# Performance work log

Hardware: AMD Instinct MI355X
Metric: run time of the kernel (lower is better)

The kernel has to match this reference:

```python
import jax, jax.numpy as jnp
import numpy as np

ITERS = 3  # iteration_num in the original module
B, L, H, N_LABELS = 16, 64, 512, 64


def setup_inputs() -> dict:
    key = jax.random.key(0)
    ks = jax.random.split(key, 11)
    s = H ** -0.5
    s2 = (2 * H) ** -0.5
    return {
        "h": jax.random.normal(ks[0], (B, L, H), jnp.float32),
        "c_slot": jax.random.normal(ks[1], (B, L, H), jnp.float32),
        "c_inte": jax.random.normal(ks[2], (B, H), jnp.float32),
        "W_SF": jax.random.normal(ks[3], (H, H), jnp.float32) * s,
        "V_SF": jax.random.normal(ks[4], (H, H), jnp.float32) * s,
        "V1_ID": jax.random.normal(ks[5], (H, H), jnp.float32) * s,
        "V2_ID_w": jax.random.normal(ks[6], (H, H), jnp.float32) * s,
        "V2_ID_b": jax.random.normal(ks[7], (H,), jnp.float32) * s,
        "W_ID": jax.random.normal(ks[8], (H, H), jnp.float32) * s,
        "W_inte_ans": jax.random.normal(ks[9], (N_LABELS, 2 * H), jnp.float32) * s2,
        "W_slot_ans": jax.random.normal(ks[10], (N_LABELS, 2 * H), jnp.float32) * s2,
    }


def reference(h, c_slot, c_inte, W_SF, V_SF, V1_ID, V2_ID_w, V2_ID_b, W_ID,
              W_inte_ans, W_slot_ans):
    # h, c_slot: [B,L,H]; c_inte: [B,H]
    # slot_features (V2_ID(h)) is loop-invariant in the original; hoisted.
    slot_features = h @ V2_ID_w.T + V2_ID_b  # [B,L,H]
    r_inte = c_inte
    r_slot = None
    for _ in range(ITERS):
        # f = sum_i V_SF(tanh(c_slot[:,i] + W_SF(r_inte))); V_SF linear -> sum first
        t = jnp.tanh(c_slot + (r_inte @ W_SF.T)[:, None, :])  # [B,L,H]
        f = t.sum(axis=1) @ V_SF.T  # [B,H]
        r_slot = f[:, None, :] * c_slot  # [B,L,H]
        hid = r_slot @ V1_ID.T  # [B,L,H]
        # pairwise additive attention scores, summed over batch AND hidden dims
        u = jnp.tanh(hid[:, :, None, :] + slot_features[:, None, :, :])  # [B,L,L,H]
        s = jnp.exp(jnp.einsum('bijh,gh->bijg', u, W_ID)).sum(axis=(0, 3))  # [L,L]
        atts = jnp.diagonal(s) / s.sum(axis=1)  # [L], scalar per position
        r = jnp.einsum('i,bih->bh', atts, r_slot)  # [B,H]
        r_inte = r + c_inte
    intent_output = jnp.concatenate([r_inte, h[:, -1, :]], axis=1) @ W_inte_ans.T  # [B,n_labels]
    slot_output = jnp.concatenate([h, r_slot], axis=-1) @ W_slot_ans.T  # [B,L,n_labels]
    return intent_output, slot_output
```

## Files before the change

### kernel.cpp

```cpp
#include <hip/hip_runtime.h>
#include <math.h>


typedef __attribute__((ext_vector_type(8))) short bf16x8;
typedef __attribute__((ext_vector_type(4))) float f32x4;

__device__ inline short f2bf(float x) {
  unsigned u = __float_as_uint(x);
  unsigned r = (u + 0x7fffu + ((u >> 16) & 1u)) >> 16;
  return (short)r;
}
__device__ inline float bf2f(short s) {
  return __uint_as_float(((unsigned)(unsigned short)s) << 16);
}
__device__ inline unsigned pack2(float a, float b) {
  return (__float_as_uint(a) >> 16) | (__float_as_uint(b) & 0xffff0000u);
}
__device__ inline float ftanh(float x) {
  float t = __expf(2.f * x);
  return 1.f - 2.f * __builtin_amdgcn_rcpf(t + 1.f);
}

__global__ __launch_bounds__(256) void k_prep(
    const float* __restrict__ W_ID, const float* __restrict__ V2,
    const float* __restrict__ V1, const float* __restrict__ W_ia,
    const float* __restrict__ W_sa, short* __restrict__ wbp,
    short* __restrict__ v2h, short* __restrict__ v2l,
    short* __restrict__ v1h, short* __restrict__ v1l,
    float* __restrict__ wia_t, float* __restrict__ wsa_t) {
  const int bx = blockIdx.x;
  const int t = threadIdx.x;
  if (bx < 1024) {
    int idx = bx * 256 + t;
    int j = idx & 7, lane = (idx >> 3) & 63;
    int ntile = (idx >> 9) & 31, kstep = idx >> 14;
    int g = ntile * 16 + (lane & 15);
    int h = kstep * 32 + (lane >> 4) * 8 + j;
    int src = g * 512 + h;
    wbp[idx] = f2bf(W_ID[src]);
    float x2 = V2[src];
    short h2 = f2bf(x2);
    v2h[idx] = h2;
    v2l[idx] = f2bf(x2 - bf2f(h2));
    float x1 = V1[src];
    short h1 = f2bf(x1);
    v1h[idx] = h1;
    v1l[idx] = f2bf(x1 - bf2f(h1));
  } else {
    const float* tin;
    float* tout;
    int c0;
    if (bx < 1040) { tin = W_ia; tout = wia_t; c0 = (bx - 1024) * 64; }
    else           { tin = W_sa; tout = wsa_t; c0 = (bx - 1040) * 64; }
    __shared__ float tile[64][65];
    const int tx = t & 63, ty = t >> 6;
#pragma unroll
    for (int it2 = 0; it2 < 16; ++it2) {
      int rl = ty + it2 * 4;
      tile[rl][tx] = tin[rl * 1024 + c0 + tx];
    }
    __syncthreads();
#pragma unroll
    for (int it2 = 0; it2 < 16; ++it2) {
      int cl = ty + it2 * 4;
      tout[(c0 + cl) * 64 + tx] = tile[tx][cl];
    }
  }
}

__global__ __launch_bounds__(256) void k_lin(const float* __restrict__ A,
                                             const float* __restrict__ c_slot,
                                             const float* __restrict__ f,
                                             const short* __restrict__ bh,
                                             const short* __restrict__ bl,
                                             const float* __restrict__ bias,
                                             float* __restrict__ C,
                                             float* __restrict__ rs_out,
                                             float* __restrict__ smat0,
                                             float* __restrict__ fzero) {
  __shared__ short Ah[2][512], Al[2][512];
  __shared__ float fl[512];
  const int m0 = blockIdx.x * 16;
  const int nh = blockIdx.y;
  const int t = threadIdx.x;
  if (smat0 && nh == 0 && blockIdx.x < 8) {
    smat0[blockIdx.x * 512 + t] = 0.f;
    smat0[blockIdx.x * 512 + 256 + t] = 0.f;
  }
  if (fzero && nh == 1 && blockIdx.x < 16) {
    fzero[blockIdx.x * 512 + t] = 0.f;
    fzero[blockIdx.x * 512 + 256 + t] = 0.f;
  }
  if (f) {
    fl[t] = f[(blockIdx.x >> 2) * 512 + t];
    fl[t + 256] = f[(blockIdx.x >> 2) * 512 + 256 + t];
  }
  const int w = t >> 6, lane = t & 63;
  const int lq = lane >> 4, lm = lane & 15;
  f32x4 acc[2];
#pragma unroll
  for (int c = 0; c < 2; ++c) acc[c] = (f32x4){0.f, 0.f, 0.f, 0.f};

  const bf16x8* gbh = (const bf16x8*)bh + (nh * 8 + w * 2) * 64 + lane;
  const bf16x8* gbl = (const bf16x8*)bl + (nh * 8 + w * 2) * 64 + lane;

  const int la = t >> 2, j0 = (t & 3) * 2;
  const int m = la & 15, kk = (la >> 4) * 8 + j0;
  const float* abase = (f ? c_slot : A) + (m0 + m) * 512 + kk;
  float* rbase = rs_out + (m0 + m) * 512 + kk;
  if (f) __syncthreads();
  float2 x = *(const float2*)abase;

  for (int ks = 0; ks < 16; ++ks) {
    const int buf = ks & 1;
    bf16x8 b0h = gbh[ks * 2048];
    bf16x8 b1h = gbh[ks * 2048 + 64];
    bf16x8 b0l = gbl[ks * 2048];
    bf16x8 b1l = gbl[ks * 2048 + 64];
    float2 xn = x;
    if (ks < 15) xn = *(const float2*)(abase + (ks + 1) * 32);
    float a0 = x.x, a1 = x.y;
    if (f) {
      a0 *= fl[ks * 32 + kk];
      a1 *= fl[ks * 32 + kk + 1];
      if (nh == 0) *(float2*)(rbase + ks * 32) = make_float2(a0, a1);
    }
    short h0 = f2bf(a0), h1 = f2bf(a1);
    short l0 = f2bf(a0 - bf2f(h0)), l1 = f2bf(a1 - bf2f(h1));
    *(short2*)&Ah[buf][t * 2] = make_short2(h0, h1);
    *(short2*)&Al[buf][t * 2] = make_short2(l0, l1);
    __syncthreads();
    bf16x8 ah = *(const bf16x8*)&Ah[buf][lane * 8];
    bf16x8 al = *(const bf16x8*)&Al[buf][lane * 8];
    acc[0] = __builtin_amdgcn_mfma_f32_16x16x32_bf16(ah, b0h, acc[0], 0, 0, 0);
    acc[0] = __builtin_amdgcn_mfma_f32_16x16x32_bf16(al, b0h, acc[0], 0, 0, 0);
    acc[0] = __builtin_amdgcn_mfma_f32_16x16x32_bf16(ah, b0l, acc[0], 0, 0, 0);
    acc[1] = __builtin_amdgcn_mfma_f32_16x16x32_bf16(ah, b1h, acc[1], 0, 0, 0);
    acc[1] = __builtin_amdgcn_mfma_f32_16x16x32_bf16(al, b1h, acc[1], 0, 0, 0);
    acc[1] = __builtin_amdgcn_mfma_f32_16x16x32_bf16(ah, b1l, acc[1], 0, 0, 0);
    x = xn;
  }
#pragma unroll
  for (int c = 0; c < 2; ++c)
#pragma unroll
    for (int reg = 0; reg < 4; ++reg) {
      int mm = m0 + lq * 4 + reg;
      int n = nh * 128 + (w * 2 + c) * 16 + lm;
      float v = acc[c][reg];
      if (bias) v += bias[n];
      C[mm * 512 + n] = v;
    }
}

__global__ __launch_bounds__(512) void k_mid(int first,
                                             const float* __restrict__ smat,
                                             const float* __restrict__ r_slot,
                                             const float* __restrict__ c_inte,
                                             const float* __restrict__ c_slot,
                                             const float* __restrict__ W_SF,
                                             const float* __restrict__ V_SF,
                                             float* __restrict__ f) {
  __shared__ float av[64];
  __shared__ float rl[512];
  __shared__ float red[512];
  __shared__ float tm[128];
  __shared__ float ts[128];
  const int b = blockIdx.x >> 2, q = blockIdx.x & 3;
  const int t = threadIdx.x;

  if (first) {
    rl[t] = c_inte[b * 512 + t];
    __syncthreads();
  } else {
    if (t < 256) {
      int w = t >> 6, lane = t & 63;
      for (int r = w * 16; r < w * 16 + 16; ++r) {
        float v = smat[r * 64 + lane];
        float s = v;
        s += __shfl_xor(s, 1);
        s += __shfl_xor(s, 2);
        s += __shfl_xor(s, 4);
        s += __shfl_xor(s, 8);
        s += __shfl_xor(s, 16);
        s += __shfl_xor(s, 32);
        float d = __shfl(v, r);
        if (lane == 0) av[r] = d / s;
      }
    }
    __syncthreads();
    float a = 0.f;
    const float* rp = r_slot + b * 64 * 512 + t;
#pragma unroll 8
    for (int i = 0; i < 64; ++i) a += av[i] * rp[i * 512];
    rl[t] = a + c_inte[b * 512 + t];
    __syncthreads();
  }

  {
    const int hh = q * 128 + (t >> 2), kq = t & 3;
    const float* wr = W_SF + hh * 512 + kq * 128;
    const float* rv = rl + kq * 128;
    float p = 0.f;
    for (int k = 0; k < 128; k += 4) {
      float4 wv = *(const float4*)(wr + k);
      p += rv[k] * wv.x + rv[k + 1] * wv.y + rv[k + 2] * wv.z + rv[k + 3] * wv.w;
    }
    red[t] = p;
  }
  __syncthreads();
  if (t < 128) tm[t] = red[t * 4] + red[t * 4 + 1] + red[t * 4 + 2] + red[t * 4 + 3];
  __syncthreads();
  {
    const int hh = q * 128 + (t >> 2), lc = t & 3;
    float tmp_h = tm[t >> 2];
    const float* cp = c_slot + (b * 64 + lc * 16) * 512 + hh;
    float s = 0.f;
    for (int l = 0; l < 16; ++l) s += ftanh(cp[l * 512] + tmp_h);
    red[t] = s;
  }
  __syncthreads();
  if (t < 128) ts[t] = red[t * 4] + red[t * 4 + 1] + red[t * 4 + 2] + red[t * 4 + 3];
  __syncthreads();
  {
    const float* vr = V_SF + t * 512 + q * 128;
    float p = 0.f;
    for (int k = 0; k < 128; k += 4) {
      float4 vv = *(const float4*)(vr + k);
      p += ts[k] * vv.x + ts[k + 1] * vv.y + ts[k + 2] * vv.z + ts[k + 3] * vv.w;
    }
    atomicAdd(&f[b * 512 + t], p);
  }
}

__global__ __launch_bounds__(512, 4) void k_score(const float* __restrict__ hid,
                                                  const float* __restrict__ sf,
                                                  const short* __restrict__ wbp,
                                                  float* __restrict__ smat,
                                                  float* __restrict__ fz,
                                                  float* __restrict__ oz) {
  __shared__ short As[16][2048];
  __shared__ float red[8][64];
  const int i = blockIdx.x, b = blockIdx.y;
  const int t = threadIdx.x;
  if (fz && i == 0) fz[b * 512 + t] = 0.f;
  if (oz && i == 1 && b < 2) oz[b * 512 + t] = 0.f;
  const int w = t >> 6, lane = t & 63;
  const int lq = lane >> 4, lm = lane & 15;

  f32x4 acc[4][4];
#pragma unroll
  for (int r = 0; r < 4; ++r)
#pragma unroll
    for (int c = 0; c < 4; ++c) acc[r][c] = (f32x4){0.f, 0.f, 0.f, 0.f};

  const float* hrow = hid + (b * 64 + i) * 512;
  const float* sfb = sf + b * 64 * 512;

  const int fid = t >> 1, half = t & 1;
  const int am = (fid >> 6) * 16 + (fid & 15);
  const int ak = ((fid >> 4) & 3) * 8 + half * 4;
  const int aoff = fid * 8 + half * 4;

  const float* hp0 = hrow + ak;
  const float* sp0 = sfb + am * 512 + ak;

#pragma unroll 4
  for (int ks = 0; ks < 16; ++ks) {
    float4 hv = *(const float4*)(hp0 + ks * 32);
    float4 sv = *(const float4*)(sp0 + ks * 32);
    uint2 pk;
    pk.x = pack2(ftanh(hv.x + sv.x), ftanh(hv.y + sv.y));
    pk.y = pack2(ftanh(hv.z + sv.z), ftanh(hv.w + sv.w));
    *(uint2*)&As[ks][aoff] = pk;
  }
  __syncthreads();

  const bf16x8* gb = (const bf16x8*)wbp + (w * 4) * 64 + lane;
  bf16x8 nb0 = gb[0];
  bf16x8 nb1 = gb[64];
  bf16x8 nb2 = gb[128];
  bf16x8 nb3 = gb[192];
  for (int ks = 0; ks < 16; ++ks) {
    bf16x8 b0 = nb0, b1 = nb1, b2 = nb2, b3 = nb3;
    if (ks < 15) {
      nb0 = gb[(ks + 1) * 2048];
      nb1 = gb[(ks + 1) * 2048 + 64];
      nb2 = gb[(ks + 1) * 2048 + 128];
      nb3 = gb[(ks + 1) * 2048 + 192];
    }
    bf16x8 af0 = *(const bf16x8*)&As[ks][(0 * 64 + lane) * 8];
    bf16x8 af1 = *(const bf16x8*)&As[ks][(1 * 64 + lane) * 8];
    bf16x8 af2 = *(const bf16x8*)&As[ks][(2 * 64 + lane) * 8];
    bf16x8 af3 = *(const bf16x8*)&As[ks][(3 * 64 + lane) * 8];
    acc[0][0] = __builtin_amdgcn_mfma_f32_16x16x32_bf16(af0, b0, acc[0][0], 0, 0, 0);
    acc[1][0] = __builtin_amdgcn_mfma_f32_16x16x32_bf16(af1, b0, acc[1][0], 0, 0, 0);
    acc[2][0] = __builtin_amdgcn_mfma_f32_16x16x32_bf16(af2, b0, acc[2][0], 0, 0, 0);
    acc[3][0] = __builtin_amdgcn_mfma_f32_16x16x32_bf16(af3, b0, acc[3][0], 0, 0, 0);
    acc[0][1] = __builtin_amdgcn_mfma_f32_16x16x32_bf16(af0, b1, acc[0][1], 0, 0, 0);
    acc[1][1] = __builtin_amdgcn_mfma_f32_16x16x32_bf16(af1, b1, acc[1][1], 0, 0, 0);
    acc[2][1] = __builtin_amdgcn_mfma_f32_16x16x32_bf16(af2, b1, acc[2][1], 0, 0, 0);
    acc[3][1] = __builtin_amdgcn_mfma_f32_16x16x32_bf16(af3, b1, acc[3][1], 0, 0, 0);
    acc[0][2] = __builtin_amdgcn_mfma_f32_16x16x32_bf16(af0, b2, acc[0][2], 0, 0, 0);
    acc[1][2] = __builtin_amdgcn_mfma_f32_16x16x32_bf16(af1, b2, acc[1][2], 0, 0, 0);
    acc[2][2] = __builtin_amdgcn_mfma_f32_16x16x32_bf16(af2, b2, acc[2][2], 0, 0, 0);
    acc[3][2] = __builtin_amdgcn_mfma_f32_16x16x32_bf16(af3, b2, acc[3][2], 0, 0, 0);
    acc[0][3] = __builtin_amdgcn_mfma_f32_16x16x32_bf16(af0, b3, acc[0][3], 0, 0, 0);
    acc[1][3] = __builtin_amdgcn_mfma_f32_16x16x32_bf16(af1, b3, acc[1][3], 0, 0, 0);
    acc[2][3] = __builtin_amdgcn_mfma_f32_16x16x32_bf16(af2, b3, acc[2][3], 0, 0, 0);
    acc[3][3] = __builtin_amdgcn_mfma_f32_16x16x32_bf16(af3, b3, acc[3][3], 0, 0, 0);
  }

#pragma unroll
  for (int r = 0; r < 4; ++r) {
#pragma unroll
    for (int reg = 0; reg < 4; ++reg) {
      float v = __expf(acc[r][0][reg]) + __expf(acc[r][1][reg]) +
                __expf(acc[r][2][reg]) + __expf(acc[r][3][reg]);
      v += __shfl_down(v, 8, 16);
      v += __shfl_down(v, 4, 16);
      v += __shfl_down(v, 2, 16);
      v += __shfl_down(v, 1, 16);
      if (lm == 0) red[w][r * 16 + lq * 4 + reg] = v;
    }
  }
  __syncthreads();
  if (t < 64) {
    float s = 0.f;
#pragma unroll
    for (int ww = 0; ww < 8; ++ww) s += red[ww][t];
    atomicAdd(&smat[i * 64 + t], s);
  }
}

__global__ __launch_bounds__(256) void k_post(const float* __restrict__ smat,
                                              const float* __restrict__ r_slot,
                                              const float* __restrict__ c_inte,
                                              const float* __restrict__ h,
                                              const float* __restrict__ wia_t,
                                              const float* __restrict__ wsa_t,
                                              float* __restrict__ out) {
  __shared__ float av[64], riv[64], red[256];
  const int t = threadIdx.x;
  if (blockIdx.x < 256) {
    int idx = blockIdx.x * 256 + t;
    int ml = idx >> 6, n = idx & 63;
    const float* x1 = h + ml * 512;
    const float* x2 = r_slot + ml * 512;
    float acc = 0.f;
    for (int k = 0; k < 512; k += 4) {
      float4 x = *(const float4*)(x1 + k);
      acc += x.x * wsa_t[k * 64 + n] + x.y * wsa_t[(k + 1) * 64 + n] +
             x.z * wsa_t[(k + 2) * 64 + n] + x.w * wsa_t[(k + 3) * 64 + n];
    }
    for (int k = 0; k < 512; k += 4) {
      float4 x = *(const float4*)(x2 + k);
      acc += x.x * wsa_t[(512 + k) * 64 + n] + x.y * wsa_t[(513 + k) * 64 + n] +
             x.z * wsa_t[(514 + k) * 64 + n] + x.w * wsa_t[(515 + k) * 64 + n];
    }
    out[1024 + idx] = acc;
  } else {
    const int bb = blockIdx.x - 256;
    const int b = bb >> 3, kc = bb & 7;
    const int w = t >> 6, lane = t & 63;
    for (int r = w * 16; r < w * 16 + 16; ++r) {
      float v = smat[r * 64 + lane];
      float s = v;
      s += __shfl_xor(s, 1);
      s += __shfl_xor(s, 2);
      s += __shfl_xor(s, 4);
      s += __shfl_xor(s, 8);
      s += __shfl_xor(s, 16);
      s += __shfl_xor(s, 32);
      float d = __shfl(v, r);
      if (lane == 0) av[r] = d / s;
    }
    __syncthreads();
    {
      const int hh = kc * 64 + lane;
      float a = 0.f;
      const float* rp = r_slot + (b * 64 + w * 16) * 512 + hh;
#pragma unroll
      for (int i = 0; i < 16; ++i) a += av[w * 16 + i] * rp[i * 512];
      red[t] = a;
    }
    __syncthreads();
    if (t < 64)
      riv[t] = red[t] + red[t + 64] + red[t + 128] + red[t + 192] +
               c_inte[b * 512 + kc * 64 + t];
    __syncthreads();
    {
      const int n = lane;
      const float* hrow = h + (b * 64 + 63) * 512 + kc * 64;
      float p = 0.f;
#pragma unroll
      for (int k = w * 16; k < w * 16 + 16; ++k) {
        p += riv[k] * wia_t[(kc * 64 + k) * 64 + n];
        p += hrow[k] * wia_t[(512 + kc * 64 + k) * 64 + n];
      }
      red[t] = p;
    }
    __syncthreads();
    if (t < 64)
      atomicAdd(&out[b * 64 + t],
                red[t] + red[t + 64] + red[t + 128] + red[t + 192]);
  }
}

extern "C" void kernel_launch(void* const* d_in, const int* in_sizes, int n_in,
                              void* d_out, int out_size, void* d_ws, size_t ws_size,
                              hipStream_t stream) {
  const float* h      = (const float*)d_in[0];
  const float* c_slot = (const float*)d_in[1];
  const float* c_inte = (const float*)d_in[2];
  const float* W_SF   = (const float*)d_in[3];
  const float* V_SF   = (const float*)d_in[4];
  const float* V1_ID  = (const float*)d_in[5];
  const float* V2_w   = (const float*)d_in[6];
  const float* V2_b   = (const float*)d_in[7];
  const float* W_ID   = (const float*)d_in[8];
  const float* W_ia   = (const float*)d_in[9];
  const float* W_sa   = (const float*)d_in[10];
  float* out = (float*)d_out;

  float* ws     = (float*)d_ws;
  short* wbp    = (short*)ws;
  short* v2h    = (short*)(ws + 131072);
  short* v2l    = (short*)(ws + 262144);
  short* v1h    = (short*)(ws + 393216);
  short* v1l    = (short*)(ws + 524288);
  float* sfbuf  = ws + 655360;
  float* r_slot = ws + 1179648;
  float* hid    = ws + 1703936;
  float* smat   = ws + 2228224;
  float* f      = ws + 2232320;
  float* wia_t  = ws + 2240512;
  float* wsa_t  = ws + 2306048;

  k_prep<<<1056, 256, 0, stream>>>(W_ID, V2_w, V1_ID, W_ia, W_sa,
                                   wbp, v2h, v2l, v1h, v1l, wia_t, wsa_t);
  k_lin<<<dim3(64, 4), 256, 0, stream>>>(h, nullptr, nullptr, v2h, v2l, V2_b,
                                         sfbuf, r_slot, nullptr, f);

  for (int it = 0; it < 3; ++it) {
    k_mid<<<64, 512, 0, stream>>>(it == 0 ? 1 : 0, smat, r_slot, c_inte,
                                  c_slot, W_SF, V_SF, f);
    k_lin<<<dim3(64, 4), 256, 0, stream>>>(nullptr, c_slot, f, v1h, v1l,
                                           nullptr, hid, r_slot, smat, nullptr);
    k_score<<<dim3(64, 16), 512, 0, stream>>>(hid, sfbuf, wbp, smat, f,
                                              it == 2 ? out : nullptr);
  }

  k_post<<<384, 256, 0, stream>>>(smat, r_slot, c_inte, h, wia_t, wsa_t, out);
}
```

Before: 337.9 us.

## Pre-transpose W_SF/V_SF and split k_mid over 8 hidden chunks per batch

```diff
diff --git a/kernel.cpp b/kernel.cpp
--- a/kernel.cpp
+++ b/kernel.cpp
@@ -24,10 +24,12 @@
 __global__ __launch_bounds__(256) void k_prep(
     const float* __restrict__ W_ID, const float* __restrict__ V2,
     const float* __restrict__ V1, const float* __restrict__ W_ia,
-    const float* __restrict__ W_sa, short* __restrict__ wbp,
+    const float* __restrict__ W_sa, const float* __restrict__ W_SF,
+    const float* __restrict__ V_SF, short* __restrict__ wbp,
     short* __restrict__ v2h, short* __restrict__ v2l,
     short* __restrict__ v1h, short* __restrict__ v1l,
-    float* __restrict__ wia_t, float* __restrict__ wsa_t) {
+    float* __restrict__ wia_t, float* __restrict__ wsa_t,
+    float* __restrict__ wsf_t, float* __restrict__ vsf_t) {
   const int bx = blockIdx.x;
   const int t = threadIdx.x;
   if (bx < 1024) {
@@ -49,21 +51,34 @@
   } else {
     const float* tin;
     float* tout;
-    int c0;
-    if (bx < 1040) { tin = W_ia; tout = wia_t; c0 = (bx - 1024) * 64; }
-    else           { tin = W_sa; tout = wsa_t; c0 = (bx - 1040) * 64; }
+    int R, C, c0, r0;
+    if (bx < 1040) {
+      tin = W_ia; tout = wia_t; R = 64; C = 1024;
+      c0 = (bx - 1024) * 64; r0 = 0;
+    } else if (bx < 1056) {
+      tin = W_sa; tout = wsa_t; R = 64; C = 1024;
+      c0 = (bx - 1040) * 64; r0 = 0;
+    } else if (bx < 1120) {
+      int bxx = bx - 1056;
+      tin = W_SF; tout = wsf_t; R = 512; C = 512;
+      c0 = (bxx & 7) * 64; r0 = (bxx >> 3) * 64;
+    } else {
+      int bxx = bx - 1120;
+      tin = V_SF; tout = vsf_t; R = 512; C = 512;
+      c0 = (bxx & 7) * 64; r0 = (bxx >> 3) * 64;
+    }
     __shared__ float tile[64][65];
     const int tx = t & 63, ty = t >> 6;
 #pragma unroll
     for (int it2 = 0; it2 < 16; ++it2) {
       int rl = ty + it2 * 4;
-      tile[rl][tx] = tin[rl * 1024 + c0 + tx];
+      tile[rl][tx] = tin[(r0 + rl) * C + c0 + tx];
     }
     __syncthreads();
 #pragma unroll
     for (int it2 = 0; it2 < 16; ++it2) {
       int cl = ty + it2 * 4;
-      tout[(c0 + cl) * 64 + tx] = tile[tx][cl];
+      tout[(c0 + cl) * R + r0 + tx] = tile[tx][cl];
     }
   }
 }
@@ -157,20 +172,19 @@
                                              const float* __restrict__ r_slot,
                                              const float* __restrict__ c_inte,
                                              const float* __restrict__ c_slot,
-                                             const float* __restrict__ W_SF,
-                                             const float* __restrict__ V_SF,
+                                             const float* __restrict__ wsf_t,
+                                             const float* __restrict__ vsf_t,
                                              float* __restrict__ f) {
   __shared__ float av[64];
-  __shared__ float rl[512];
+  __shared__ float riv[512];
   __shared__ float red[512];
-  __shared__ float tm[128];
-  __shared__ float ts[128];
-  const int b = blockIdx.x >> 2, q = blockIdx.x & 3;
+  __shared__ float tm[64], ts[64];
+  const int b = blockIdx.x >> 3, hc = blockIdx.x & 7;
   const int t = threadIdx.x;
+  const int hl = t & 63, kq = t >> 6;
 
   if (first) {
-    rl[t] = c_inte[b * 512 + t];
-    __syncthreads();
+    riv[t] = c_inte[b * 512 + t];
   } else {
     if (t < 256) {
       int w = t >> 6, lane = t & 63;
@@ -192,42 +206,45 @@
     const float* rp = r_slot + b * 64 * 512 + t;
 #pragma unroll 8
     for (int i = 0; i < 64; ++i) a += av[i] * rp[i * 512];
-    rl[t] = a + c_inte[b * 512 + t];
-    __syncthreads();
-  }
-
+    riv[t] = a + c_inte[b * 512 + t];
+  }
+  __syncthreads();
   {
-    const int hh = q * 128 + (t >> 2), kq = t & 3;
-    const float* wr = W_SF + hh * 512 + kq * 128;
-    const float* rv = rl + kq * 128;
+    const float* wp = wsf_t + hc * 64 + hl;
     float p = 0.f;
-    for (int k = 0; k < 128; k += 4) {
-      float4 wv = *(const float4*)(wr + k);
-      p += rv[k] * wv.x + rv[k + 1] * wv.y + rv[k + 2] * wv.z + rv[k + 3] * wv.w;
-    }
+#pragma unroll 8
+    for (int k = kq * 64; k < kq * 64 + 64; ++k) p += riv[k] * wp[k * 512];
     red[t] = p;
   }
   __syncthreads();
-  if (t < 128) tm[t] = red[t * 4] + red[t * 4 + 1] + red[t * 4 + 2] + red[t * 4 + 3];
+  if (t < 64) {
+    float s = 0.f;
+#pragma unroll
+    for (int q = 0; q < 8; ++q) s += red[q * 64 + t];
+    tm[t] = s;
+  }
   __syncthreads();
   {
-    const int hh = q * 128 + (t >> 2), lc = t & 3;
-    float tmp_h = tm[t >> 2];
-    const float* cp = c_slot + (b * 64 + lc * 16) * 512 + hh;
+    float tmph = tm[hl];
+    const float* cp = c_slot + (b * 64 + kq * 8) * 512 + hc * 64 + hl;
     float s = 0.f;
-    for (int l = 0; l < 16; ++l) s += ftanh(cp[l * 512] + tmp_h);
+#pragma unroll
+    for (int l = 0; l < 8; ++l) s += ftanh(cp[l * 512] + tmph);
     red[t] = s;
   }
   __syncthreads();
-  if (t < 128) ts[t] = red[t * 4] + red[t * 4 + 1] + red[t * 4 + 2] + red[t * 4 + 3];
+  if (t < 64) {
+    float s = 0.f;
+#pragma unroll
+    for (int q = 0; q < 8; ++q) s += red[q * 64 + t];
+    ts[t] = s;
+  }
   __syncthreads();
   {
-    const float* vr = V_SF + t * 512 + q * 128;
+    const float* vp = vsf_t + (hc * 64) * 512 + t;
     float p = 0.f;
-    for (int k = 0; k < 128; k += 4) {
-      float4 vv = *(const float4*)(vr + k);
-      p += ts[k] * vv.x + ts[k + 1] * vv.y + ts[k + 2] * vv.z + ts[k + 3] * vv.w;
-    }
+#pragma unroll 8
+    for (int k = 0; k < 64; ++k) p += ts[k] * vp[k * 512];
     atomicAdd(&f[b * 512 + t], p);
   }
 }
@@ -435,15 +452,18 @@
   float* f      = ws + 2232320;
   float* wia_t  = ws + 2240512;
   float* wsa_t  = ws + 2306048;
-
-  k_prep<<<1056, 256, 0, stream>>>(W_ID, V2_w, V1_ID, W_ia, W_sa,
-                                   wbp, v2h, v2l, v1h, v1l, wia_t, wsa_t);
+  float* wsf_t  = ws + 2371584;
+  float* vsf_t  = ws + 2633728;
+
+  k_prep<<<1184, 256, 0, stream>>>(W_ID, V2_w, V1_ID, W_ia, W_sa, W_SF, V_SF,
+                                   wbp, v2h, v2l, v1h, v1l,
+                                   wia_t, wsa_t, wsf_t, vsf_t);
   k_lin<<<dim3(64, 4), 256, 0, stream>>>(h, nullptr, nullptr, v2h, v2l, V2_b,
                                          sfbuf, r_slot, nullptr, f);
 
   for (int it = 0; it < 3; ++it) {
-    k_mid<<<64, 512, 0, stream>>>(it == 0 ? 1 : 0, smat, r_slot, c_inte,
-                                  c_slot, W_SF, V_SF, f);
+    k_mid<<<128, 512, 0, stream>>>(it == 0 ? 1 : 0, smat, r_slot, c_inte,
+                                   c_slot, wsf_t, vsf_t, f);
     k_lin<<<dim3(64, 4), 256, 0, stream>>>(nullptr, c_slot, f, v1h, v1l,
                                            nullptr, hid, r_slot, smat, nullptr);
     k_score<<<dim3(64, 16), 512, 0, stream>>>(hid, sfbuf, wbp, smat, f,
```

After: 306.3 us. -9.4%, faster.
